# Kernel tuning notes

Hardware: AMD Instinct MI355X
Metric: run time of the kernel (lower is better)

The kernel has to match this reference:

```python
import jax, jax.numpy as jnp
import numpy as np

B_, L_, H_, P_ = 8, 4096, 512, 256
DT_LO, DT_HI = 1e-3, 4e-3  # keep Heinsen log-space weights in fp32 range for L=4096


def setup_inputs() -> dict:
    key = jax.random.key(0)
    ks = jax.random.split(key, 8)
    u = jax.random.normal(ks[0], (B_, L_, H_), dtype=jnp.float32)
    # Diagonal continuous-time state matrix Lambda (HiPPO-N-like: Re=-0.5, structured imag parts)
    lambda_re = -0.5 * jnp.ones((P_,), dtype=jnp.float32)
    lambda_im = jnp.pi * (jnp.arange(P_, dtype=jnp.float32) + 1.0)
    # Input/output projections (complex, stored as re/im pairs)
    B_re = jax.random.normal(ks[1], (P_, H_), dtype=jnp.float32) / jnp.sqrt(float(H_))
    B_im = jax.random.normal(ks[2], (P_, H_), dtype=jnp.float32) / jnp.sqrt(float(H_))
    C_re = jax.random.normal(ks[3], (H_, P_), dtype=jnp.float32) / jnp.sqrt(float(P_))
    C_im = jax.random.normal(ks[4], (H_, P_), dtype=jnp.float32) / jnp.sqrt(float(P_))
    D = jax.random.normal(ks[5], (H_,), dtype=jnp.float32)
    # Per-state learnable log-timescales, log-uniform in [DT_LO, DT_HI]
    log_delta = jax.random.uniform(ks[6], (P_,), dtype=jnp.float32,
                                   minval=jnp.log(DT_LO), maxval=jnp.log(DT_HI))
    return {"u": u, "lambda_re": lambda_re, "lambda_im": lambda_im,
            "B_re": B_re, "B_im": B_im, "C_re": C_re, "C_im": C_im,
            "D": D, "log_delta": log_delta}


def reference(u, lambda_re, lambda_im, B_re, B_im, C_re, C_im, D, log_delta):
    # --- ZOH discretization (eq. 6 of S5 paper) ---
    lam = lambda_re + 1j * lambda_im                     # (P,) complex64
    delta = jnp.exp(log_delta)                           # (P,)
    lambda_bar = jnp.exp(lam * delta)                    # (P,) complex
    B_tilde = B_re + 1j * B_im                           # (P,H)
    B_bar = ((lambda_bar - 1.0) / lam)[:, None] * B_tilde  # (P,H)

    # --- input projection: Bu_k = B_bar @ u_k ---
    Bu = jnp.einsum('blh,ph->blp', u.astype(B_bar.dtype), B_bar)  # (B,L,P) complex

    # --- Heinsen log-space parallel scan: x_k = lambda_bar * x_{k-1} + Bu_k ---
    L = u.shape[1]
    log_lambda = jnp.log(lambda_bar)                     # (P,) complex
    k = jnp.arange(L, dtype=jnp.float32)
    weights = jnp.exp(k[:, None] * log_lambda[None, :])  # (L,P) complex
    xs = weights[None] * jnp.cumsum(Bu / weights[None], axis=1)  # (B,L,P)

    # --- output: y_k = 2*Re(C_tilde x_k) + D*u_k (conjugate symmetry) ---
    C_tilde = C_re + 1j * C_im                           # (H,P)
    y = 2.0 * jnp.real(jnp.einsum('blp,hp->blh', xs, C_tilde)) + D * u
    return y
```

## Files before the change

### kernel.cpp

```cpp
#include <hip/hip_runtime.h>
#include <math.h>

#define HH 512
#define PP 256
#define LSEQ 4096
#define BB 8
#define MTOT (BB*LSEQ)
#define N2P 512

typedef __attribute__((ext_vector_type(8))) short bf16x8;
typedef __attribute__((ext_vector_type(4))) float f32x4;
typedef __attribute__((ext_vector_type(8))) unsigned short u16x8;
typedef __attribute__((ext_vector_type(4))) unsigned short u16x4;

__device__ inline unsigned short f2bf(float f) {
    union { float f; unsigned int u; } v; v.f = f;
    unsigned int u = v.u;
    u += 0x7fffu + ((u >> 16) & 1u);
    return (unsigned short)(u >> 16);
}
__device__ inline float bf2f(unsigned short h) {
    union { unsigned int u; float f; } v; v.u = ((unsigned int)h) << 16;
    return v.f;
}

#define SWZ(row) (((((row) & 7) ^ (((row) >> 3) & 7)) << 4))

__global__ void prep_w1_k(const float* __restrict__ lre, const float* __restrict__ lim,
                          const float* __restrict__ logd,
                          const float* __restrict__ Bre, const float* __restrict__ Bim,
                          unsigned short* __restrict__ W1t, float2* __restrict__ lamb) {
    int idx = blockIdx.x * 256 + threadIdx.x;
    if (idx >= PP * HH) return;
    int p = idx >> 9;
    int h = idx & (HH - 1);
    float delta = expf(logd[p]);
    float lr = lre[p], li = lim[p];
    float er = expf(lr * delta);
    float th = li * delta;
    float lbr = er * cosf(th), lbi = er * sinf(th);
    if (h == 0) lamb[p] = make_float2(lbr, lbi);
    float a = lbr - 1.0f, b = lbi;
    float n2 = lr * lr + li * li;
    float gr = (a * lr + b * li) / n2;
    float gi = (b * lr - a * li) / n2;
    float br = Bre[idx], bi = Bim[idx];
    W1t[(size_t)p * HH + h]        = f2bf(gr * br - gi * bi);
    W1t[(size_t)(PP + p) * HH + h] = f2bf(gr * bi + gi * br);
}

__global__ void prep_w2_k(const float* __restrict__ Cre, const float* __restrict__ Cim,
                          unsigned short* __restrict__ W2t) {
    int idx = blockIdx.x * 256 + threadIdx.x;
    if (idx >= HH * N2P) return;
    int h = idx >> 9;
    int k = idx & 511;
    float v = (k < PP) ? 2.0f * Cre[(size_t)h * PP + k]
                       : -2.0f * Cim[(size_t)h * PP + (k - PP)];
    W2t[(size_t)h * N2P + k] = f2bf(v);
}

__global__ __launch_bounds__(256) void gemm1_k(const float* __restrict__ u,
                                               const unsigned short* __restrict__ W1t,
                                               unsigned short* __restrict__ T1) {
    __shared__ char smem[32768];
    char* Asw = smem;
    char* Bsw = smem + 16384;
    const int tid = threadIdx.x;
    const int m0 = blockIdx.y * 128;
    const int n0 = blockIdx.x * 128;
    const int wave = tid >> 6, lane = tid & 63;
    const int wm = (wave >> 1) * 64, wn = (wave & 1) * 64;

    f32x4 acc[4][4] = {};

    for (int k0 = 0; k0 < 512; k0 += 64) {
        #pragma unroll
        for (int it = 0; it < 4; ++it) {
            int idx = it * 256 + tid;
            int row = idx >> 3, c = idx & 7;
            const float4 v0 = *(const float4*)&u[(size_t)(m0 + row) * HH + k0 + c * 8];
            const float4 v1 = *(const float4*)&u[(size_t)(m0 + row) * HH + k0 + c * 8 + 4];
            bf16x8 pk;
            pk[0] = (short)f2bf(v0.x); pk[1] = (short)f2bf(v0.y);
            pk[2] = (short)f2bf(v0.z); pk[3] = (short)f2bf(v0.w);
            pk[4] = (short)f2bf(v1.x); pk[5] = (short)f2bf(v1.y);
            pk[6] = (short)f2bf(v1.z); pk[7] = (short)f2bf(v1.w);
            *(bf16x8*)(Asw + row * 128 + ((c * 16) ^ SWZ(row))) = pk;
        }
        #pragma unroll
        for (int it = 0; it < 4; ++it) {
            int idx = it * 256 + tid;
            int row = idx >> 3, c = idx & 7;
            bf16x8 pk = *(const bf16x8*)&W1t[(size_t)(n0 + row) * HH + k0 + c * 8];
            *(bf16x8*)(Bsw + row * 128 + ((c * 16) ^ SWZ(row))) = pk;
        }
        __syncthreads();

        bf16x8 af[4][2], bfr[4][2];
        #pragma unroll
        for (int f = 0; f < 4; ++f) {
            #pragma unroll
            for (int kk = 0; kk < 2; ++kk) {
                int ar = wm + f * 16 + (lane & 15);
                af[f][kk]  = *(const bf16x8*)(Asw + ar * 128 + ((kk * 64 + (lane >> 4) * 16) ^ SWZ(ar)));
                int br = wn + f * 16 + (lane & 15);
                bfr[f][kk] = *(const bf16x8*)(Bsw + br * 128 + ((kk * 64 + (lane >> 4) * 16) ^ SWZ(br)));
            }
        }
        #pragma unroll
        for (int fm = 0; fm < 4; ++fm)
            #pragma unroll
            for (int fn = 0; fn < 4; ++fn)
                #pragma unroll
                for (int kk = 0; kk < 2; ++kk)
                    acc[fm][fn] = __builtin_amdgcn_mfma_f32_16x16x32_bf16(
                        af[fm][kk], bfr[fn][kk], acc[fm][fn], 0, 0, 0);
        __syncthreads();
    }

    #pragma unroll
    for (int fm = 0; fm < 4; ++fm) {
        #pragma unroll
        for (int fn = 0; fn < 4; ++fn) {
            int r = n0 + wn + fn * 16 + (lane & 15);
            int m = m0 + wm + fm * 16 + ((lane >> 4) << 2);
            u16x4 pk;
            pk[0] = f2bf(acc[fm][fn][0]); pk[1] = f2bf(acc[fm][fn][1]);
            pk[2] = f2bf(acc[fm][fn][2]); pk[3] = f2bf(acc[fm][fn][3]);
            *(u16x4*)&T1[(size_t)r * MTOT + m] = pk;
        }
    }
}

__global__ __launch_bounds__(256) void gemm2_k(const unsigned short* __restrict__ Xs,
                                               const unsigned short* __restrict__ W2t,
                                               float* __restrict__ y,
                                               const float* __restrict__ u,
                                               const float* __restrict__ D) {
    __shared__ char smem[65536];
    char* Asw = smem;
    char* Bsw = smem + 16384;
    float* epi = (float*)smem;
    const int tid = threadIdx.x;
    const int m0 = blockIdx.y * 128;
    const int n0 = blockIdx.x * 128;
    const int wave = tid >> 6, lane = tid & 63;
    const int wm = (wave >> 1) * 64, wn = (wave & 1) * 64;

    f32x4 acc[4][4] = {};

    for (int k0 = 0; k0 < 512; k0 += 64) {
        #pragma unroll
        for (int it = 0; it < 4; ++it) {
            int idx = it * 256 + tid;
            int kr = idx >> 4, c = idx & 15;
            u16x8 v = *(const u16x8*)&Xs[(size_t)(k0 + kr) * MTOT + m0 + c * 8];
            #pragma unroll
            for (int j = 0; j < 8; ++j) {
                int m = c * 8 + j;
                *(unsigned short*)(Asw + m * 128 + ((kr * 2) ^ SWZ(m))) = v[j];
            }
        }
        #pragma unroll
        for (int it = 0; it < 4; ++it) {
            int idx = it * 256 + tid;
            int row = idx >> 3, c = idx & 7;
            bf16x8 pk = *(const bf16x8*)&W2t[(size_t)(n0 + row) * N2P + k0 + c * 8];
            *(bf16x8*)(Bsw + row * 128 + ((c * 16) ^ SWZ(row))) = pk;
        }
        __syncthreads();

        bf16x8 af[4][2], bfr[4][2];
        #pragma unroll
        for (int f = 0; f < 4; ++f) {
            #pragma unroll
            for (int kk = 0; kk < 2; ++kk) {
                int ar = wm + f * 16 + (lane & 15);
                af[f][kk]  = *(const bf16x8*)(Asw + ar * 128 + ((kk * 64 + (lane >> 4) * 16) ^ SWZ(ar)));
                int br = wn + f * 16 + (lane & 15);
                bfr[f][kk] = *(const bf16x8*)(Bsw + br * 128 + ((kk * 64 + (lane >> 4) * 16) ^ SWZ(br)));
            }
        }
        #pragma unroll
        for (int fm = 0; fm < 4; ++fm)
            #pragma unroll
            for (int fn = 0; fn < 4; ++fn)
                #pragma unroll
                for (int kk = 0; kk < 2; ++kk)
                    acc[fm][fn] = __builtin_amdgcn_mfma_f32_16x16x32_bf16(
                        af[fm][kk], bfr[fn][kk], acc[fm][fn], 0, 0, 0);
        __syncthreads();
    }

    float* myepi = epi + wave * 4096;
    #pragma unroll
    for (int fm = 0; fm < 4; ++fm) {
        #pragma unroll
        for (int fn = 0; fn < 4; ++fn) {
            int ml = fm * 16 + ((lane >> 4) << 2);
            int hl = fn * 16 + (lane & 15);
            #pragma unroll
            for (int i = 0; i < 4; ++i)
                myepi[(ml + i) * 64 + hl] = acc[fm][fn][i];
        }
    }
    __syncthreads();

    #pragma unroll
    for (int it = 0; it < 16; ++it) {
        int idx = it * 256 + tid;
        int ml = idx >> 5, c = idx & 31;
        int w = ((ml >> 6) << 1) + (c >> 4);
        const float4 v = *(const float4*)(epi + w * 4096 + (ml & 63) * 64 + (c & 15) * 4);
        int grow = m0 + ml, gcol = n0 + c * 4;
        const float4 uv = *(const float4*)&u[(size_t)grow * HH + gcol];
        const float4 dv = *(const float4*)&D[gcol];
        float4 o = make_float4(v.x + dv.x * uv.x, v.y + dv.y * uv.y,
                               v.z + dv.z * uv.z, v.w + dv.w * uv.w);
        *(float4*)&y[(size_t)grow * HH + gcol] = o;
    }
}

__global__ __launch_bounds__(256) void scan_k(const unsigned short* __restrict__ T1,
                                              unsigned short* __restrict__ Xs,
                                              const float2* __restrict__ lamb) {
    const int b = blockIdx.x >> 8;
    const int p = blockIdx.x & 255;
    const int t = threadIdx.x;
    const float2 L = lamb[p];

    const size_t baseRe = (size_t)p * MTOT + (size_t)b * LSEQ + t * 16;
    const size_t baseIm = (size_t)(PP + p) * MTOT + (size_t)b * LSEQ + t * 16;

    u16x8 r0 = *(const u16x8*)&T1[baseRe];
    u16x8 r1 = *(const u16x8*)&T1[baseRe + 8];
    u16x8 i0 = *(const u16x8*)&T1[baseIm];
    u16x8 i1 = *(const u16x8*)&T1[baseIm + 8];

    float re[16], im[16];
    #pragma unroll
    for (int j = 0; j < 8; ++j) {
        re[j] = bf2f(r0[j]); re[8 + j] = bf2f(r1[j]);
        im[j] = bf2f(i0[j]); im[8 + j] = bf2f(i1[j]);
    }

    float sr = 0.f, si = 0.f;
    #pragma unroll
    for (int j = 0; j < 16; ++j) {
        float nsr = L.x * sr - L.y * si + re[j];
        si = L.x * si + L.y * sr + im[j];
        sr = nsr;
    }

    __shared__ float cr[256], ci[256];
    cr[t] = sr; ci[t] = si;
    __syncthreads();

    float wr = L.x, wi = L.y;
    #pragma unroll
    for (int q = 0; q < 4; ++q) { float nr = wr * wr - wi * wi; wi = 2.f * wr * wi; wr = nr; }

    for (int off = 1; off < 256; off <<= 1) {
        float pr = 0.f, pi = 0.f;
        const bool has = (t >= off);
        if (has) { pr = cr[t - off]; pi = ci[t - off]; }
        __syncthreads();
        if (has) {
            sr += wr * pr - wi * pi;
            si += wr * pi + wi * pr;
            cr[t] = sr; ci[t] = si;
        }
        __syncthreads();
        float nr = wr * wr - wi * wi; wi = 2.f * wr * wi; wr = nr;
    }

    float xr = 0.f, xi = 0.f;
    if (t > 0) { xr = cr[t - 1]; xi = ci[t - 1]; }

    u16x8 o0, o1, o2, o3;
    #pragma unroll
    for (int j = 0; j < 16; ++j) {
        float nr = L.x * xr - L.y * xi + re[j];
        xi = L.x * xi + L.y * xr + im[j];
        xr = nr;
        if (j < 8) { o0[j] = f2bf(xr); o2[j] = f2bf(xi); }
        else       { o1[j - 8] = f2bf(xr); o3[j - 8] = f2bf(xi); }
    }
    *(u16x8*)&Xs[baseRe]     = o0;
    *(u16x8*)&Xs[baseRe + 8] = o1;
    *(u16x8*)&Xs[baseIm]     = o2;
    *(u16x8*)&Xs[baseIm + 8] = o3;
}


extern "C" void kernel_launch(void* const* d_in, const int* in_sizes, int n_in,
                              void* d_out, int out_size, void* d_ws, size_t ws_size,
                              hipStream_t stream) {
    const float* u    = (const float*)d_in[0];
    const float* lre  = (const float*)d_in[1];
    const float* lim  = (const float*)d_in[2];
    const float* Bre  = (const float*)d_in[3];
    const float* Bim  = (const float*)d_in[4];
    const float* Cre  = (const float*)d_in[5];
    const float* Cim  = (const float*)d_in[6];
    const float* Dv   = (const float*)d_in[7];
    const float* logd = (const float*)d_in[8];
    float* out = (float*)d_out;

    char* ws = (char*)d_ws;
    unsigned short* W1t  = (unsigned short*)ws;
    unsigned short* W2t  = (unsigned short*)(ws + (512 << 10));
    float2*         lamb = (float2*)(ws + (1 << 20));
    unsigned short* Xs   = (unsigned short*)(ws + (1 << 20) + 4096);

    unsigned short* T1 = (unsigned short*)d_out;

    prep_w1_k<<<(PP * HH) / 256, 256, 0, stream>>>(lre, lim, logd, Bre, Bim, W1t, lamb);
    prep_w2_k<<<(HH * N2P) / 256, 256, 0, stream>>>(Cre, Cim, W2t);

    gemm1_k<<<dim3(N2P / 128, MTOT / 128), 256, 0, stream>>>(u, W1t, T1);
    scan_k<<<BB * PP, 256, 0, stream>>>(T1, Xs, lamb);
    gemm2_k<<<dim3(HH / 128, MTOT / 128), 256, 0, stream>>>(Xs, W2t, out, u, Dv);
}
```

Before: 121.3 us.

## Double-buffer GEMM K-loop with direct global-to-LDS weight loads and pre-swizzled panels

Both GEMM kernels now double-buffer their LDS tiles. The next K-slice is prefetched into registers, with weight panels copied straight to LDS via global_load_lds, while MFMAs run on the current slice. The prep kernels write weights in a pre-swizzled 128x64 panel layout so the LDS copy is a contiguous 16-byte-per-lane stream. The grid is also remapped to a 1D order for better L2 locality, and gemm2's transpose writes go from scalar shorts to u16x4. The cost is twice the LDS footprint (64KB), which may lower occupancy, plus more register pressure from the prefetch buffers.

Result: faster. 97.63 us (-19.5%).

```diff
diff --git a/kernel.cpp b/kernel.cpp
--- a/kernel.cpp
+++ b/kernel.cpp
@@ -1,4 +1,5 @@
 #include <hip/hip_runtime.h>
+#include <hip/hip_bf16.h>
 #include <math.h>
 
 #define HH 512
@@ -13,23 +14,31 @@
 typedef __attribute__((ext_vector_type(8))) unsigned short u16x8;
 typedef __attribute__((ext_vector_type(4))) unsigned short u16x4;
 
-__device__ inline unsigned short f2bf(float f) {
-    union { float f; unsigned int u; } v; v.f = f;
-    unsigned int u = v.u;
-    u += 0x7fffu + ((u >> 16) & 1u);
-    return (unsigned short)(u >> 16);
-}
-__device__ inline float bf2f(unsigned short h) {
+#define SWZ(row) (((((row) & 7) ^ (((row) >> 3) & 7)) << 4))
+
+__device__ inline unsigned short f2b(float x) {
+    return __builtin_bit_cast(unsigned short, __float2bfloat16(x));
+}
+__device__ inline float b2f(unsigned short h) {
     union { unsigned int u; float f; } v; v.u = ((unsigned int)h) << 16;
     return v.f;
 }
 
-#define SWZ(row) (((((row) & 7) ^ (((row) >> 3) & 7)) << 4))
+#define GLOAD16(gp, lp) __builtin_amdgcn_global_load_lds( \
+    (const __attribute__((address_space(1))) unsigned int*)(gp), \
+    (__attribute__((address_space(3))) unsigned int*)(lp), 16, 0, 0)
+
+__device__ inline size_t panel_off(int r, int k) {
+    int nblk = r >> 7, rl = r & 127;
+    int kblk = k >> 6, kl = k & 63;
+    int c = kl >> 3, j = kl & 7;
+    return (size_t)(nblk * 8 + kblk) * 16384 + rl * 128 + ((c * 16) ^ SWZ(rl)) + j * 2;
+}
 
 __global__ void prep_w1_k(const float* __restrict__ lre, const float* __restrict__ lim,
                           const float* __restrict__ logd,
                           const float* __restrict__ Bre, const float* __restrict__ Bim,
-                          unsigned short* __restrict__ W1t, float2* __restrict__ lamb) {
+                          char* __restrict__ W1s, float2* __restrict__ lamb) {
     int idx = blockIdx.x * 256 + threadIdx.x;
     if (idx >= PP * HH) return;
     int p = idx >> 9;
@@ -45,77 +54,84 @@
     float gr = (a * lr + b * li) / n2;
     float gi = (b * lr - a * li) / n2;
     float br = Bre[idx], bi = Bim[idx];
-    W1t[(size_t)p * HH + h]        = f2bf(gr * br - gi * bi);
-    W1t[(size_t)(PP + p) * HH + h] = f2bf(gr * bi + gi * br);
+    *(unsigned short*)(W1s + panel_off(p, h))      = f2b(gr * br - gi * bi);
+    *(unsigned short*)(W1s + panel_off(PP + p, h)) = f2b(gr * bi + gi * br);
 }
 
 __global__ void prep_w2_k(const float* __restrict__ Cre, const float* __restrict__ Cim,
-                          unsigned short* __restrict__ W2t) {
+                          char* __restrict__ W2s) {
     int idx = blockIdx.x * 256 + threadIdx.x;
     if (idx >= HH * N2P) return;
     int h = idx >> 9;
     int k = idx & 511;
     float v = (k < PP) ? 2.0f * Cre[(size_t)h * PP + k]
                        : -2.0f * Cim[(size_t)h * PP + (k - PP)];
-    W2t[(size_t)h * N2P + k] = f2bf(v);
-}
+    *(unsigned short*)(W2s + panel_off(h, k)) = f2b(v);
+}
+
+#define TILE_COMPUTE(ABUF, BBUF) { \
+    bf16x8 af[4][2], bfr[4][2]; \
+    _Pragma("unroll") for (int f = 0; f < 4; ++f) { \
+      _Pragma("unroll") for (int kk = 0; kk < 2; ++kk) { \
+        int ar = wm + f * 16 + (lane & 15); \
+        af[f][kk]  = *(const bf16x8*)((ABUF) + ar * 128 + ((kk * 64 + (lane >> 4) * 16) ^ SWZ(ar))); \
+        int br = wn + f * 16 + (lane & 15); \
+        bfr[f][kk] = *(const bf16x8*)((BBUF) + br * 128 + ((kk * 64 + (lane >> 4) * 16) ^ SWZ(br))); } } \
+    _Pragma("unroll") for (int fm = 0; fm < 4; ++fm) { \
+      _Pragma("unroll") for (int fn = 0; fn < 4; ++fn) { \
+        _Pragma("unroll") for (int kk = 0; kk < 2; ++kk) { \
+          acc[fm][fn] = __builtin_amdgcn_mfma_f32_16x16x32_bf16(af[fm][kk], bfr[fn][kk], acc[fm][fn], 0, 0, 0); } } } }
 
 __global__ __launch_bounds__(256) void gemm1_k(const float* __restrict__ u,
-                                               const unsigned short* __restrict__ W1t,
+                                               const char* __restrict__ W1s,
                                                unsigned short* __restrict__ T1) {
-    __shared__ char smem[32768];
-    char* Asw = smem;
-    char* Bsw = smem + 16384;
-    const int tid = threadIdx.x;
-    const int m0 = blockIdx.y * 128;
-    const int n0 = blockIdx.x * 128;
-    const int wave = tid >> 6, lane = tid & 63;
+    __shared__ char smem[65536];
+    const int tid = threadIdx.x, wave = tid >> 6, lane = tid & 63;
+    const int swz = (blockIdx.x & 7) * 128 + (blockIdx.x >> 3);
+    const int m0 = (swz >> 2) * 128;
+    const int nblk = swz & 3, n0 = nblk * 128;
     const int wm = (wave >> 1) * 64, wn = (wave & 1) * 64;
-
+    const int arow = tid >> 3, acol = tid & 7;
+
+    float4 av0[4], av1[4];
     f32x4 acc[4][4] = {};
 
-    for (int k0 = 0; k0 < 512; k0 += 64) {
-        #pragma unroll
-        for (int it = 0; it < 4; ++it) {
-            int idx = it * 256 + tid;
-            int row = idx >> 3, c = idx & 7;
-            const float4 v0 = *(const float4*)&u[(size_t)(m0 + row) * HH + k0 + c * 8];
-            const float4 v1 = *(const float4*)&u[(size_t)(m0 + row) * HH + k0 + c * 8 + 4];
-            bf16x8 pk;
-            pk[0] = (short)f2bf(v0.x); pk[1] = (short)f2bf(v0.y);
-            pk[2] = (short)f2bf(v0.z); pk[3] = (short)f2bf(v0.w);
-            pk[4] = (short)f2bf(v1.x); pk[5] = (short)f2bf(v1.y);
-            pk[6] = (short)f2bf(v1.z); pk[7] = (short)f2bf(v1.w);
-            *(bf16x8*)(Asw + row * 128 + ((c * 16) ^ SWZ(row))) = pk;
-        }
-        #pragma unroll
-        for (int it = 0; it < 4; ++it) {
-            int idx = it * 256 + tid;
-            int row = idx >> 3, c = idx & 7;
-            bf16x8 pk = *(const bf16x8*)&W1t[(size_t)(n0 + row) * HH + k0 + c * 8];
-            *(bf16x8*)(Bsw + row * 128 + ((c * 16) ^ SWZ(row))) = pk;
-        }
-        __syncthreads();
-
-        bf16x8 af[4][2], bfr[4][2];
-        #pragma unroll
-        for (int f = 0; f < 4; ++f) {
-            #pragma unroll
-            for (int kk = 0; kk < 2; ++kk) {
-                int ar = wm + f * 16 + (lane & 15);
-                af[f][kk]  = *(const bf16x8*)(Asw + ar * 128 + ((kk * 64 + (lane >> 4) * 16) ^ SWZ(ar)));
-                int br = wn + f * 16 + (lane & 15);
-                bfr[f][kk] = *(const bf16x8*)(Bsw + br * 128 + ((kk * 64 + (lane >> 4) * 16) ^ SWZ(br)));
-            }
-        }
-        #pragma unroll
-        for (int fm = 0; fm < 4; ++fm)
-            #pragma unroll
-            for (int fn = 0; fn < 4; ++fn)
-                #pragma unroll
-                for (int kk = 0; kk < 2; ++kk)
-                    acc[fm][fn] = __builtin_amdgcn_mfma_f32_16x16x32_bf16(
-                        af[fm][kk], bfr[fn][kk], acc[fm][fn], 0, 0, 0);
+#define G1_A_LOAD(K0) { \
+    _Pragma("unroll") for (int it = 0; it < 4; ++it) { \
+        int row = it * 32 + arow; \
+        const float* src = &u[(size_t)(m0 + row) * HH + (K0) + acol * 8]; \
+        av0[it] = *(const float4*)src; av1[it] = *(const float4*)(src + 4); } }
+
+#define G1_A_WRITE(ABUF) { \
+    _Pragma("unroll") for (int it = 0; it < 4; ++it) { \
+        int row = it * 32 + arow; \
+        bf16x8 pk; \
+        pk[0] = (short)f2b(av0[it].x); pk[1] = (short)f2b(av0[it].y); \
+        pk[2] = (short)f2b(av0[it].z); pk[3] = (short)f2b(av0[it].w); \
+        pk[4] = (short)f2b(av1[it].x); pk[5] = (short)f2b(av1[it].y); \
+        pk[6] = (short)f2b(av1[it].z); pk[7] = (short)f2b(av1[it].w); \
+        *(bf16x8*)((ABUF) + row * 128 + ((acol * 16) ^ SWZ(row))) = pk; } }
+
+#define G1_B_GLOAD(K0, BBUF) { \
+    const char* panel = W1s + (size_t)(nblk * 8 + ((K0) >> 6)) * 16384 + wave * 4096 + lane * 16; \
+    _Pragma("unroll") for (int q = 0; q < 4; ++q) \
+        GLOAD16(panel + q * 1024, (BBUF) + wave * 4096 + q * 1024); }
+
+    char* A0 = smem;          char* B0 = smem + 16384;
+    char* A1 = smem + 32768;  char* B1 = smem + 49152;
+
+    G1_A_LOAD(0); G1_B_GLOAD(0, B0); G1_A_WRITE(A0);
+    asm volatile("s_waitcnt vmcnt(0)" ::: "memory");
+    __syncthreads();
+
+    #pragma unroll
+    for (int t = 0; t < 8; ++t) {
+        char* Ac = (t & 1) ? A1 : A0; char* Bc = (t & 1) ? B1 : B0;
+        char* An = (t & 1) ? A0 : A1; char* Bn = (t & 1) ? B0 : B1;
+        if (t < 7) { G1_A_LOAD((t + 1) * 64); G1_B_GLOAD((t + 1) * 64, Bn); }
+        TILE_COMPUTE(Ac, Bc);
+        if (t < 7) { G1_A_WRITE(An); }
+        asm volatile("s_waitcnt vmcnt(0)" ::: "memory");
         __syncthreads();
     }
 
@@ -126,73 +142,63 @@
             int r = n0 + wn + fn * 16 + (lane & 15);
             int m = m0 + wm + fm * 16 + ((lane >> 4) << 2);
             u16x4 pk;
-            pk[0] = f2bf(acc[fm][fn][0]); pk[1] = f2bf(acc[fm][fn][1]);
-            pk[2] = f2bf(acc[fm][fn][2]); pk[3] = f2bf(acc[fm][fn][3]);
+            pk[0] = f2b(acc[fm][fn][0]); pk[1] = f2b(acc[fm][fn][1]);
+            pk[2] = f2b(acc[fm][fn][2]); pk[3] = f2b(acc[fm][fn][3]);
             *(u16x4*)&T1[(size_t)r * MTOT + m] = pk;
         }
     }
 }
 
 __global__ __launch_bounds__(256) void gemm2_k(const unsigned short* __restrict__ Xs,
-                                               const unsigned short* __restrict__ W2t,
+                                               const char* __restrict__ W2s,
                                                float* __restrict__ y,
                                                const float* __restrict__ u,
                                                const float* __restrict__ D) {
     __shared__ char smem[65536];
-    char* Asw = smem;
-    char* Bsw = smem + 16384;
+    const int tid = threadIdx.x, wave = tid >> 6, lane = tid & 63;
+    const int swz = (blockIdx.x & 7) * 128 + (blockIdx.x >> 3);
+    const int m0 = (swz >> 2) * 128;
+    const int nblk = swz & 3, n0 = nblk * 128;
+    const int wm = (wave >> 1) * 64, wn = (wave & 1) * 64;
+    const int kg = tid >> 4, mc = tid & 15;
+
+    u16x8 xv[4];
+    f32x4 acc[4][4] = {};
+
+#define G2_A_LOAD(K0) { \
+    _Pragma("unroll") for (int kk = 0; kk < 4; ++kk) \
+        xv[kk] = *(const u16x8*)&Xs[(size_t)((K0) + kg * 4 + kk) * MTOT + m0 + mc * 8]; }
+
+#define G2_A_WRITE(ABUF) { \
+    _Pragma("unroll") for (int j = 0; j < 8; ++j) { \
+        int row = mc * 8 + j; \
+        u16x4 o; o[0] = xv[0][j]; o[1] = xv[1][j]; o[2] = xv[2][j]; o[3] = xv[3][j]; \
+        *(u16x4*)((ABUF) + row * 128 + ((kg * 8) ^ SWZ(row))) = o; } }
+
+#define G2_B_GLOAD(K0, BBUF) { \
+    const char* panel = W2s + (size_t)(nblk * 8 + ((K0) >> 6)) * 16384 + wave * 4096 + lane * 16; \
+    _Pragma("unroll") for (int q = 0; q < 4; ++q) \
+        GLOAD16(panel + q * 1024, (BBUF) + wave * 4096 + q * 1024); }
+
+    char* A0 = smem;          char* B0 = smem + 16384;
+    char* A1 = smem + 32768;  char* B1 = smem + 49152;
+
+    G2_A_LOAD(0); G2_B_GLOAD(0, B0); G2_A_WRITE(A0);
+    asm volatile("s_waitcnt vmcnt(0)" ::: "memory");
+    __syncthreads();
+
+    #pragma unroll
+    for (int t = 0; t < 8; ++t) {
+        char* Ac = (t & 1) ? A1 : A0; char* Bc = (t & 1) ? B1 : B0;
+        char* An = (t & 1) ? A0 : A1; char* Bn = (t & 1) ? B0 : B1;
+        if (t < 7) { G2_A_LOAD((t + 1) * 64); G2_B_GLOAD((t + 1) * 64, Bn); }
+        TILE_COMPUTE(Ac, Bc);
+        if (t < 7) { G2_A_WRITE(An); }
+        asm volatile("s_waitcnt vmcnt(0)" ::: "memory");
+        __syncthreads();
+    }
+
     float* epi = (float*)smem;
-    const int tid = threadIdx.x;
-    const int m0 = blockIdx.y * 128;
-    const int n0 = blockIdx.x * 128;
-    const int wave = tid >> 6, lane = tid & 63;
-    const int wm = (wave >> 1) * 64, wn = (wave & 1) * 64;
-
-    f32x4 acc[4][4] = {};
-
-    for (int k0 = 0; k0 < 512; k0 += 64) {
-        #pragma unroll
-        for (int it = 0; it < 4; ++it) {
-            int idx = it * 256 + tid;
-            int kr = idx >> 4, c = idx & 15;
-            u16x8 v = *(const u16x8*)&Xs[(size_t)(k0 + kr) * MTOT + m0 + c * 8];
-            #pragma unroll
-            for (int j = 0; j < 8; ++j) {
-                int m = c * 8 + j;
-                *(unsigned short*)(Asw + m * 128 + ((kr * 2) ^ SWZ(m))) = v[j];
-            }
-        }
-        #pragma unroll
-        for (int it = 0; it < 4; ++it) {
-            int idx = it * 256 + tid;
-            int row = idx >> 3, c = idx & 7;
-            bf16x8 pk = *(const bf16x8*)&W2t[(size_t)(n0 + row) * N2P + k0 + c * 8];
-            *(bf16x8*)(Bsw + row * 128 + ((c * 16) ^ SWZ(row))) = pk;
-        }
-        __syncthreads();
-
-        bf16x8 af[4][2], bfr[4][2];
-        #pragma unroll
-        for (int f = 0; f < 4; ++f) {
-            #pragma unroll
-            for (int kk = 0; kk < 2; ++kk) {
-                int ar = wm + f * 16 + (lane & 15);
-                af[f][kk]  = *(const bf16x8*)(Asw + ar * 128 + ((kk * 64 + (lane >> 4) * 16) ^ SWZ(ar)));
-                int br = wn + f * 16 + (lane & 15);
-                bfr[f][kk] = *(const bf16x8*)(Bsw + br * 128 + ((kk * 64 + (lane >> 4) * 16) ^ SWZ(br)));
-            }
-        }
-        #pragma unroll
-        for (int fm = 0; fm < 4; ++fm)
-            #pragma unroll
-            for (int fn = 0; fn < 4; ++fn)
-                #pragma unroll
-                for (int kk = 0; kk < 2; ++kk)
-                    acc[fm][fn] = __builtin_amdgcn_mfma_f32_16x16x32_bf16(
-                        af[fm][kk], bfr[fn][kk], acc[fm][fn], 0, 0, 0);
-        __syncthreads();
-    }
-
     float* myepi = epi + wave * 4096;
     #pragma unroll
     for (int fm = 0; fm < 4; ++fm) {
@@ -241,8 +247,8 @@
     float re[16], im[16];
     #pragma unroll
     for (int j = 0; j < 8; ++j) {
-        re[j] = bf2f(r0[j]); re[8 + j] = bf2f(r1[j]);
-        im[j] = bf2f(i0[j]); im[8 + j] = bf2f(i1[j]);
+        re[j] = b2f(r0[j]); re[8 + j] = b2f(r1[j]);
+        im[j] = b2f(i0[j]); im[8 + j] = b2f(i1[j]);
     }
 
     float sr = 0.f, si = 0.f;
@@ -284,8 +290,8 @@
         float nr = L.x * xr - L.y * xi + re[j];
         xi = L.x * xi + L.y * xr + im[j];
         xr = nr;
-        if (j < 8) { o0[j] = f2bf(xr); o2[j] = f2bf(xi); }
-        else       { o1[j - 8] = f2bf(xr); o3[j - 8] = f2bf(xi); }
+        if (j < 8) { o0[j] = f2b(xr); o2[j] = f2b(xi); }
+        else       { o1[j - 8] = f2b(xr); o3[j - 8] = f2b(xi); }
     }
     *(u16x8*)&Xs[baseRe]     = o0;
     *(u16x8*)&Xs[baseRe + 8] = o1;
@@ -309,17 +315,17 @@
     float* out = (float*)d_out;
 
     char* ws = (char*)d_ws;
-    unsigned short* W1t  = (unsigned short*)ws;
-    unsigned short* W2t  = (unsigned short*)(ws + (512 << 10));
+    char*           W1s  = ws;
+    char*           W2s  = ws + (512 << 10);
     float2*         lamb = (float2*)(ws + (1 << 20));
     unsigned short* Xs   = (unsigned short*)(ws + (1 << 20) + 4096);
 
     unsigned short* T1 = (unsigned short*)d_out;
 
-    prep_w1_k<<<(PP * HH) / 256, 256, 0, stream>>>(lre, lim, logd, Bre, Bim, W1t, lamb);
-    prep_w2_k<<<(HH * N2P) / 256, 256, 0, stream>>>(Cre, Cim, W2t);
-
-    gemm1_k<<<dim3(N2P / 128, MTOT / 128), 256, 0, stream>>>(u, W1t, T1);
+    prep_w1_k<<<(PP * HH) / 256, 256, 0, stream>>>(lre, lim, logd, Bre, Bim, W1s, lamb);
+    prep_w2_k<<<(HH * N2P) / 256, 256, 0, stream>>>(Cre, Cim, W2s);
+
+    gemm1_k<<<1024, 256, 0, stream>>>(u, W1s, T1);
     scan_k<<<BB * PP, 256, 0, stream>>>(T1, Xs, lamb);
-    gemm2_k<<<dim3(HH / 128, MTOT / 128), 256, 0, stream>>>(Xs, W2t, out, u, Dv);
-}
+    gemm2_k<<<1024, 256, 0, stream>>>(Xs, W2s, out, u, Dv);
+}
```
